# Kernel optimization log

Measured on AMD Instinct MI355X. Metric: run time of the kernel, lower is better.

The kernel has to match this reference:

```python
import jax, jax.numpy as jnp
import numpy as np

B, T, C = 2, 2048, 1024
H, HS = 16, 64
THETA = 10000.0


def _rope_tables(seq_len, dim, dtype):
    inv_freq = 1.0 / (THETA ** (jnp.arange(0, dim, 2, dtype=jnp.float32) / dim))
    t = jnp.arange(seq_len, dtype=jnp.float32)
    freqs = t[:, None] * inv_freq[None, :]          # [T, dim/2]
    emb = jnp.concatenate([freqs, freqs], axis=-1)  # [T, dim]
    return jnp.cos(emb).astype(dtype), jnp.sin(emb).astype(dtype)


def _rotate_half(x):
    x1, x2 = jnp.split(x, 2, axis=-1)
    return jnp.concatenate([-x2, x1], axis=-1)


def setup_inputs() -> dict:
    key = jax.random.key(0)
    ks = jax.random.split(key, 9)
    s = 0.02
    return {
        "q_x": jax.random.normal(ks[0], (B, T, C), dtype=jnp.float32),
        "wq": jax.random.normal(ks[1], (C, H * HS), dtype=jnp.float32) * s,
        "bq": jnp.zeros((H * HS,), dtype=jnp.float32),
        "wk": jax.random.normal(ks[2], (C, H * HS), dtype=jnp.float32) * s,
        "bk": jnp.zeros((H * HS,), dtype=jnp.float32),
        "wv": jax.random.normal(ks[3], (C, H * HS), dtype=jnp.float32) * s,
        "bv": jnp.zeros((H * HS,), dtype=jnp.float32),
        "wc": jax.random.normal(ks[4], (H * HS, C), dtype=jnp.float32) * s,
        "bc": jnp.zeros((C,), dtype=jnp.float32),
    }


def reference(q_x, wq, bq, wk, bk, wv, bv, wc, bc):
    b, t, _ = q_x.shape
    # Q/K/V projections -> [B, H, T, HS]
    q = (q_x @ wq + bq).reshape(b, t, H, HS).transpose(0, 2, 1, 3)
    k = (q_x @ wk + bk).reshape(b, t, H, HS).transpose(0, 2, 1, 3)
    v = (q_x @ wv + bv).reshape(b, t, H, HS).transpose(0, 2, 1, 3)
    # RoPE (concat-half rotation)
    cos, sin = _rope_tables(t, HS, q.dtype)  # [T, HS]
    q = q * cos + _rotate_half(q) * sin
    k = k * cos + _rotate_half(k) * sin
    # Naive causal attention
    scale = 1.0 / np.sqrt(HS)
    att = jnp.einsum("bhqd,bhkd->bhqk", q, k) * scale
    mask = jnp.tril(jnp.ones((t, t), dtype=bool))
    att = jnp.where(mask, att, -jnp.inf)
    att = jax.nn.softmax(att, axis=-1)
    y = jnp.einsum("bhqk,bhkd->bhqd", att, v)
    y = y.transpose(0, 2, 1, 3).reshape(b, t, H * HS)
    return y @ wc + bc
```

## Files before the change

### kernel.cpp

```cpp
#include <hip/hip_runtime.h>

#define B_  2
#define T_  2048
#define C_  1024
#define H_  16
#define HS_ 64
#define M_  4096
#define N_  1024
#define K_  1024

typedef float floatx4 __attribute__((ext_vector_type(4)));
typedef short bf16x8  __attribute__((ext_vector_type(8)));

__device__ __forceinline__ float bf2f(unsigned short u) {
    return __uint_as_float(((unsigned int)u) << 16);
}
__device__ __forceinline__ unsigned short f2bf(float f) {
    unsigned int u = __float_as_uint(f);
    return (unsigned short)((u + 0x7fffu + ((u >> 16) & 1u)) >> 16);
}
__device__ __forceinline__ unsigned int pack2(float a, float b) {
    return (unsigned int)f2bf(a) | ((unsigned int)f2bf(b) << 16);
}
__device__ __forceinline__ void async16(const unsigned short* g, unsigned short* l) {
    __builtin_amdgcn_global_load_lds(
        (const __attribute__((address_space(1))) unsigned int*)g,
        (__attribute__((address_space(3))) unsigned int*)l, 16, 0, 0);
}

__global__ __launch_bounds__(256) void convert_x(const float* __restrict__ x,
                                                 unsigned short* __restrict__ xb)
{
    const size_t i = ((size_t)blockIdx.x * 256 + threadIdx.x) * 4;
    const float4 v = *(const float4*)(x + i);
    ushort4 st;
    st.x = f2bf(v.x); st.y = f2bf(v.y); st.z = f2bf(v.z); st.w = f2bf(v.w);
    *(ushort4*)(xb + i) = st;
}

__global__ __launch_bounds__(256) void transpose_w(
    const float* __restrict__ w0, const float* __restrict__ w1,
    const float* __restrict__ w2, const float* __restrict__ w3,
    unsigned short* __restrict__ wTall)
{
    __shared__ float tile[64][65];
    const int z = blockIdx.z;
    const float* w = (z == 0) ? w0 : (z == 1) ? w1 : (z == 2) ? w2 : w3;
    unsigned short* wT = wTall + ((size_t)z << 20);

    const int n0 = blockIdx.x * 64, k0 = blockIdx.y * 64;
    const int t = threadIdx.x;
    const int r = t >> 2, cq = (t & 3) * 16;

    const float4* src = (const float4*)(w + (size_t)(k0 + r) * N_ + n0 + cq);
    const float4 v0 = src[0], v1 = src[1], v2 = src[2], v3 = src[3];
    tile[r][cq+0]=v0.x; tile[r][cq+1]=v0.y; tile[r][cq+2]=v0.z; tile[r][cq+3]=v0.w;
    tile[r][cq+4]=v1.x; tile[r][cq+5]=v1.y; tile[r][cq+6]=v1.z; tile[r][cq+7]=v1.w;
    tile[r][cq+8]=v2.x; tile[r][cq+9]=v2.y; tile[r][cq+10]=v2.z; tile[r][cq+11]=v2.w;
    tile[r][cq+12]=v3.x; tile[r][cq+13]=v3.y; tile[r][cq+14]=v3.z; tile[r][cq+15]=v3.w;
    __syncthreads();

    const int rn = t >> 2, ck = (t & 3) * 16;
    unsigned int o[8];
#pragma unroll
    for (int ii = 0; ii < 8; ii++)
        o[ii] = pack2(tile[ck + 2*ii][rn], tile[ck + 2*ii + 1][rn]);
    unsigned short* dst = wT + (size_t)(n0 + rn) * K_ + k0 + ck;
    *(uint4*)dst       = make_uint4(o[0], o[1], o[2], o[3]);
    *(uint4*)(dst + 8) = make_uint4(o[4], o[5], o[6], o[7]);
}

__global__ __launch_bounds__(256) void qkv_gemm(
    const unsigned short* __restrict__ xb, const unsigned short* __restrict__ wT,
    const float* __restrict__ bq, const float* __restrict__ bk,
    const float* __restrict__ bv,
    unsigned short* __restrict__ qb, unsigned short* __restrict__ kb,
    unsigned short* __restrict__ vb)
{
    __shared__ unsigned short As[128 * 32];
    __shared__ unsigned short Bs[128 * 32];

    const int tid  = threadIdx.x;
    const int lane = tid & 63;
    const int wave = tid >> 6;
    const int p  = blockIdx.x >> 3;
    const int n0 = (blockIdx.x & 7) * 128;
    const int m0 = blockIdx.y * 128;
    const float* bias = (p == 0) ? bq : (p == 1) ? bk : bv;

    const int lrow = lane >> 2, lch = (lane & 3) * 8;
    const unsigned short* ag0 = xb + (size_t)(m0 + wave * 32 + lrow) * K_ + lch;
    const unsigned short* ag1 = ag0 + (size_t)16 * K_;
    const unsigned short* wb  = wT + ((size_t)p << 20);
    const unsigned short* bg0 = wb + (size_t)(n0 + wave * 32 + lrow) * K_ + lch;
    const unsigned short* bg1 = bg0 + (size_t)16 * K_;
    unsigned short* lA0 = &As[(wave * 32) * 32];
    unsigned short* lA1 = &As[(wave * 32 + 16) * 32];
    unsigned short* lB0 = &Bs[(wave * 32) * 32];
    unsigned short* lB1 = &Bs[(wave * 32 + 16) * 32];

    const int fr = lane & 15;
    const int fk = (lane >> 4) * 8;
    const int wr = wave >> 1, wc = wave & 1;

    floatx4 acc[4][4];
#pragma unroll
    for (int i = 0; i < 4; i++)
#pragma unroll
        for (int j = 0; j < 4; j++) acc[i][j] = (floatx4){0.f, 0.f, 0.f, 0.f};

    for (int k0 = 0; k0 < K_; k0 += 32) {
        __syncthreads();
        async16(ag0 + k0, lA0);
        async16(ag1 + k0, lA1);
        async16(bg0 + k0, lB0);
        async16(bg1 + k0, lB1);
        __syncthreads();

        bf16x8 af[4], bfr[4];
#pragma unroll
        for (int i = 0; i < 4; i++)
            af[i] = *(const bf16x8*)&As[(wr * 64 + i * 16 + fr) * 32 + fk];
#pragma unroll
        for (int j = 0; j < 4; j++)
            bfr[j] = *(const bf16x8*)&Bs[(wc * 64 + j * 16 + fr) * 32 + fk];
#pragma unroll
        for (int i = 0; i < 4; i++)
#pragma unroll
            for (int j = 0; j < 4; j++)
                acc[i][j] = __builtin_amdgcn_mfma_f32_16x16x32_bf16(
                    af[i], bfr[j], acc[i][j], 0, 0, 0);
    }

    const int rbase = (lane >> 4) * 4;
    if (p == 2) {
#pragma unroll
        for (int j = 0; j < 4; j++) {
            const int col = n0 + wc * 64 + j * 16 + fr;
            const float bz = bias[col];
            const int h = col >> 6, d = col & 63;
#pragma unroll
            for (int i = 0; i < 4; i++) {
                const int row0 = m0 + wr * 64 + i * 16 + rbase;
                const int bb = row0 >> 11, tt = row0 & 2047;
                ushort4 st;
                st.x = f2bf(acc[i][j][0] + bz);
                st.y = f2bf(acc[i][j][1] + bz);
                st.z = f2bf(acc[i][j][2] + bz);
                st.w = f2bf(acc[i][j][3] + bz);
                *(ushort4*)&vb[((size_t)(bb * H_ + h) * HS_ + d) * T_ + tt] = st;
            }
        }
    } else {
        unsigned short* out = (p == 0) ? qb : kb;
#pragma unroll
        for (int j = 0; j < 4; j++) {
            const int col = n0 + wc * 64 + j * 16 + fr;
            const float bz = bias[col];
            const int h = col >> 6, d = col & 63;
#pragma unroll
            for (int i = 0; i < 4; i++) {
#pragma unroll
                for (int pr = 0; pr < 4; pr++) {
                    const int row = m0 + wr * 64 + i * 16 + rbase + pr;
                    const int bb = row >> 11, tt = row & 2047;
                    out[((size_t)(bb * H_ + h) * T_ + tt) * HS_ + d] =
                        f2bf(acc[i][j][pr] + bz);
                }
            }
        }
    }
}

__global__ __launch_bounds__(256) void rope_kernel(unsigned short* __restrict__ qb,
                                                   unsigned short* __restrict__ kb)
{
    const int idx = blockIdx.x * 256 + threadIdx.x;
    const int d  = idx & 31;
    const int t  = (idx >> 5) & (T_ - 1);
    const int bh = idx >> 16;
    const size_t base = ((size_t)bh * T_ + t) * HS_;

    const float inv_freq = powf(10000.0f, -(float)d * (1.0f / 32.0f));
    float s, c;
    sincosf((float)t * inv_freq, &s, &c);

    {
        float x1 = bf2f(qb[base + d]), x2 = bf2f(qb[base + d + 32]);
        qb[base + d]      = f2bf((x1 * c - x2 * s) * 0.125f);
        qb[base + d + 32] = f2bf((x2 * c + x1 * s) * 0.125f);
    }
    {
        float x1 = bf2f(kb[base + d]), x2 = bf2f(kb[base + d + 32]);
        kb[base + d]      = f2bf(x1 * c - x2 * s);
        kb[base + d + 32] = f2bf(x2 * c + x1 * s);
    }
}

__global__ __launch_bounds__(256) void attn_kernel(
    const unsigned short* __restrict__ qb, const unsigned short* __restrict__ kb,
    const unsigned short* __restrict__ vt, unsigned short* __restrict__ yb)
{
    __shared__ unsigned short Ks[64 * 64];
    __shared__ unsigned short Vs[64 * 64];
    __shared__ unsigned short Ps[4][16 * 64];

    const int bh = blockIdx.x;
    const int b = bh >> 4, h = bh & 15;
    const int qt = blockIdx.y;
    const int r0 = qt * 64;
    const int tid  = threadIdx.x;
    const int lane = tid & 63;
    const int wave = tid >> 6;
    const int l4   = lane & 15;
    const int quad = lane >> 4;

    const int qrow_g = r0 + wave * 16 + l4;

    bf16x8 qf[2];
    {
        const unsigned short* qp = qb + ((size_t)bh * T_ + qrow_g) * HS_ + quad * 8;
        qf[0] = *(const bf16x8*)(qp);
        qf[1] = *(const bf16x8*)(qp + 32);
    }

    floatx4 o[4];
#pragma unroll
    for (int g = 0; g < 4; g++) o[g] = (floatx4){0.f, 0.f, 0.f, 0.f};
    float m = -1e30f, l = 0.f;

    const int srow = tid >> 2;
    const int sc16 = (tid & 3) * 16;
    const int ssw  = (srow & 7) * 8;
    const int psw  = (l4 & 7) * 8;

    for (int kt = 0; kt <= qt; kt++) {
        const unsigned short* kp = kb + ((size_t)bh * T_ + kt * 64 + srow) * HS_ + sc16;
        const uint4 k0 = *(const uint4*)kp;
        const uint4 k1 = *(const uint4*)(kp + 8);
        const unsigned short* vp = vt + ((size_t)(bh * 64 + srow)) * T_ + kt * 64 + sc16;
        const uint4 v0 = *(const uint4*)vp;
        const uint4 v1 = *(const uint4*)(vp + 8);

        __syncthreads();
        *(uint4*)&Ks[srow * 64 + ( sc16      ^ ssw)] = k0;
        *(uint4*)&Ks[srow * 64 + ((sc16 + 8) ^ ssw)] = k1;
        *(uint4*)&Vs[srow * 64 + ( sc16      ^ ssw)] = v0;
        *(uint4*)&Vs[srow * 64 + ((sc16 + 8) ^ ssw)] = v1;
        __syncthreads();

        floatx4 sf[4];
#pragma unroll
        for (int mg = 0; mg < 4; mg++) {
            const int key = mg * 16 + l4;
            const int ksw = (key & 7) * 8;
            const bf16x8 a0 = *(const bf16x8*)&Ks[key * 64 + ( (quad * 8)       ^ ksw)];
            const bf16x8 a1 = *(const bf16x8*)&Ks[key * 64 + (((quad * 8) + 32) ^ ksw)];
            floatx4 z = (floatx4){0.f, 0.f, 0.f, 0.f};
            z = __builtin_amdgcn_mfma_f32_16x16x32_bf16(a0, qf[0], z, 0, 0, 0);
            z = __builtin_amdgcn_mfma_f32_16x16x32_bf16(a1, qf[1], z, 0, 0, 0);
            sf[mg] = z;
        }

        if (kt == qt) {
#pragma unroll
            for (int mg = 0; mg < 4; mg++)
#pragma unroll
                for (int r = 0; r < 4; r++)
                    if (kt * 64 + 16 * mg + quad * 4 + r > qrow_g)
                        sf[mg][r] = -1e30f;
        }

        float tm = sf[0][0];
#pragma unroll
        for (int mg = 0; mg < 4; mg++)
#pragma unroll
            for (int r = 0; r < 4; r++) tm = fmaxf(tm, sf[mg][r]);
        tm = fmaxf(tm, __shfl_xor(tm, 16));
        tm = fmaxf(tm, __shfl_xor(tm, 32));
        const float mnew  = fmaxf(m, tm);
        const float alpha = __expf(m - mnew);

        float p[4][4];
        float ps = 0.f;
#pragma unroll
        for (int mg = 0; mg < 4; mg++)
#pragma unroll
            for (int r = 0; r < 4; r++) {
                p[mg][r] = __expf(sf[mg][r] - mnew);
                ps += p[mg][r];
            }
        ps += __shfl_xor(ps, 16);
        ps += __shfl_xor(ps, 32);
        l = l * alpha + ps;
        m = mnew;
#pragma unroll
        for (int g = 0; g < 4; g++) {
            o[g][0] *= alpha; o[g][1] *= alpha;
            o[g][2] *= alpha; o[g][3] *= alpha;
        }

#pragma unroll
        for (int mg = 0; mg < 4; mg++) {
            const int kb4 = 16 * mg + quad * 4;
            const int off = ((kb4 & ~7) ^ psw) | (kb4 & 7);
            uint2 w;
            w.x = pack2(p[mg][0], p[mg][1]);
            w.y = pack2(p[mg][2], p[mg][3]);
            *(uint2*)&Ps[wave][l4 * 64 + off] = w;
        }

        const bf16x8 pf0 = *(const bf16x8*)&Ps[wave][l4 * 64 + ( (quad * 8)       ^ psw)];
        const bf16x8 pf1 = *(const bf16x8*)&Ps[wave][l4 * 64 + (((quad * 8) + 32) ^ psw)];
#pragma unroll
        for (int g = 0; g < 4; g++) {
            const int vd  = g * 16 + l4;
            const int vsw = (vd & 7) * 8;
            const bf16x8 va0 = *(const bf16x8*)&Vs[vd * 64 + ( (quad * 8)       ^ vsw)];
            const bf16x8 va1 = *(const bf16x8*)&Vs[vd * 64 + (((quad * 8) + 32) ^ vsw)];
            o[g] = __builtin_amdgcn_mfma_f32_16x16x32_bf16(va0, pf0, o[g], 0, 0, 0);
            o[g] = __builtin_amdgcn_mfma_f32_16x16x32_bf16(va1, pf1, o[g], 0, 0, 0);
        }
    }

    const float invl = 1.f / l;
    unsigned short* yrow = yb + ((size_t)(b * T_ + qrow_g) * H_ + h) * HS_;
#pragma unroll
    for (int g = 0; g < 4; g++) {
        ushort4 st;
        st.x = f2bf(o[g][0] * invl);
        st.y = f2bf(o[g][1] * invl);
        st.z = f2bf(o[g][2] * invl);
        st.w = f2bf(o[g][3] * invl);
        *(ushort4*)&yrow[16 * g + quad * 4] = st;
    }
}

__global__ __launch_bounds__(256) void out_gemm(
    const unsigned short* __restrict__ A, const unsigned short* __restrict__ wcT,
    const float* __restrict__ bias, float* __restrict__ out)
{
    __shared__ unsigned short As[128 * 32];
    __shared__ unsigned short Bs[128 * 32];

    const int tid  = threadIdx.x;
    const int lane = tid & 63;
    const int wave = tid >> 6;
    const int n0 = blockIdx.x * 128;
    const int m0 = blockIdx.y * 128;

    const int lrow = lane >> 2, lch = (lane & 3) * 8;
    const unsigned short* ag0 = A + (size_t)(m0 + wave * 32 + lrow) * K_ + lch;
    const unsigned short* ag1 = ag0 + (size_t)16 * K_;
    const unsigned short* bg0 = wcT + (size_t)(n0 + wave * 32 + lrow) * K_ + lch;
    const unsigned short* bg1 = bg0 + (size_t)16 * K_;
    unsigned short* lA0 = &As[(wave * 32) * 32];
    unsigned short* lA1 = &As[(wave * 32 + 16) * 32];
    unsigned short* lB0 = &Bs[(wave * 32) * 32];
    unsigned short* lB1 = &Bs[(wave * 32 + 16) * 32];

    const int fr = lane & 15;
    const int fk = (lane >> 4) * 8;
    const int wr = wave >> 1, wc = wave & 1;

    floatx4 acc[4][4];
#pragma unroll
    for (int i = 0; i < 4; i++)
#pragma unroll
        for (int j = 0; j < 4; j++) acc[i][j] = (floatx4){0.f, 0.f, 0.f, 0.f};

    for (int k0 = 0; k0 < K_; k0 += 32) {
        __syncthreads();
        async16(ag0 + k0, lA0);
        async16(ag1 + k0, lA1);
        async16(bg0 + k0, lB0);
        async16(bg1 + k0, lB1);
        __syncthreads();

        bf16x8 af[4], bfr[4];
#pragma unroll
        for (int i = 0; i < 4; i++)
            af[i] = *(const bf16x8*)&As[(wr * 64 + i * 16 + fr) * 32 + fk];
#pragma unroll
        for (int j = 0; j < 4; j++)
            bfr[j] = *(const bf16x8*)&Bs[(wc * 64 + j * 16 + fr) * 32 + fk];
#pragma unroll
        for (int i = 0; i < 4; i++)
#pragma unroll
            for (int j = 0; j < 4; j++)
                acc[i][j] = __builtin_amdgcn_mfma_f32_16x16x32_bf16(
                    af[i], bfr[j], acc[i][j], 0, 0, 0);
    }

    const int rbase = (lane >> 4) * 4;
#pragma unroll
    for (int j = 0; j < 4; j++) {
        const int col = n0 + wc * 64 + j * 16 + fr;
        const float bz = bias[col];
#pragma unroll
        for (int i = 0; i < 4; i++) {
#pragma unroll
            for (int pr = 0; pr < 4; pr++) {
                const int row = m0 + wr * 64 + i * 16 + rbase + pr;
                out[(size_t)row * N_ + col] = acc[i][j][pr] + bz;
            }
        }
    }
}

extern "C" void kernel_launch(void* const* d_in, const int* in_sizes, int n_in,
                              void* d_out, int out_size, void* d_ws, size_t ws_size,
                              hipStream_t stream) {
    const float* x  = (const float*)d_in[0];
    const float* wq = (const float*)d_in[1];
    const float* bq = (const float*)d_in[2];
    const float* wk = (const float*)d_in[3];
    const float* bk = (const float*)d_in[4];
    const float* wv = (const float*)d_in[5];
    const float* bv = (const float*)d_in[6];
    const float* wc = (const float*)d_in[7];
    const float* bc = (const float*)d_in[8];
    float* out = (float*)d_out;

    unsigned short* ws  = (unsigned short*)d_ws;
    unsigned short* qb  = ws;
    unsigned short* kb  = ws + (size_t)4194304;
    unsigned short* vb  = ws + (size_t)8388608;
    unsigned short* yb  = ws + (size_t)12582912;
    unsigned short* xb  = ws + (size_t)16777216;
    unsigned short* wT  = ws + (size_t)20971520;
    unsigned short* wcT = wT + ((size_t)3 << 20);

    convert_x<<<4096, 256, 0, stream>>>(x, xb);
    transpose_w<<<dim3(16, 16, 4), 256, 0, stream>>>(wq, wk, wv, wc, wT);
    qkv_gemm<<<dim3(24, 32), 256, 0, stream>>>(xb, wT, bq, bk, bv, qb, kb, vb);
    rope_kernel<<<(B_ * H_ * T_ * 32) / 256, 256, 0, stream>>>(qb, kb);
    attn_kernel<<<dim3(32, 32), 256, 0, stream>>>(qb, kb, vb, yb);
    out_gemm<<<dim3(8, 32), 256, 0, stream>>>(yb, wcT, bc, out);
}
```

Baseline: 231.3 us.

## Fuse RoPE into QKV epilogue, double-buffer attention K/V, reverse tile order

```diff
diff --git a/kernel.cpp b/kernel.cpp
--- a/kernel.cpp
+++ b/kernel.cpp
@@ -133,12 +133,13 @@
     }
 
     const int rbase = (lane >> 4) * 4;
+    const int h = (n0 + wc * 64) >> 6;
     if (p == 2) {
 #pragma unroll
         for (int j = 0; j < 4; j++) {
             const int col = n0 + wc * 64 + j * 16 + fr;
             const float bz = bias[col];
-            const int h = col >> 6, d = col & 63;
+            const int d = col & 63;
 #pragma unroll
             for (int i = 0; i < 4; i++) {
                 const int row0 = m0 + wr * 64 + i * 16 + rbase;
@@ -153,47 +154,34 @@
         }
     } else {
         unsigned short* out = (p == 0) ? qb : kb;
-#pragma unroll
-        for (int j = 0; j < 4; j++) {
-            const int col = n0 + wc * 64 + j * 16 + fr;
-            const float bz = bias[col];
-            const int h = col >> 6, d = col & 63;
-#pragma unroll
-            for (int i = 0; i < 4; i++) {
-#pragma unroll
-                for (int pr = 0; pr < 4; pr++) {
-                    const int row = m0 + wr * 64 + i * 16 + rbase + pr;
-                    const int bb = row >> 11, tt = row & 2047;
-                    out[((size_t)(bb * H_ + h) * T_ + tt) * HS_ + d] =
-                        f2bf(acc[i][j][pr] + bz);
-                }
+        const float qsc = (p == 0) ? 0.18033688011111772f : 1.0f;
+        const float bz0 = bias[n0 + wc * 64 + fr];
+        const float bz1 = bias[n0 + wc * 64 + 16 + fr];
+        const float bz2 = bias[n0 + wc * 64 + 32 + fr];
+        const float bz3 = bias[n0 + wc * 64 + 48 + fr];
+        const float nl = -0.41524101186279297f;
+        const float if0 = exp2f((float)fr * nl);
+        const float if1 = exp2f((float)(fr + 16) * nl);
+#pragma unroll
+        for (int i = 0; i < 4; i++) {
+#pragma unroll
+            for (int pr = 0; pr < 4; pr++) {
+                const int row = m0 + wr * 64 + i * 16 + rbase + pr;
+                const int bb = row >> 11, tt = row & 2047;
+                float s0, c0, s1, c1;
+                __sincosf((float)tt * if0, &s0, &c0);
+                __sincosf((float)tt * if1, &s1, &c1);
+                const float v0 = acc[i][0][pr] + bz0;
+                const float v1 = acc[i][1][pr] + bz1;
+                const float v2 = acc[i][2][pr] + bz2;
+                const float v3 = acc[i][3][pr] + bz3;
+                unsigned short* ob = out + ((size_t)(bb * H_ + h) * T_ + tt) * HS_ + fr;
+                ob[0]  = f2bf((v0 * c0 - v2 * s0) * qsc);
+                ob[16] = f2bf((v1 * c1 - v3 * s1) * qsc);
+                ob[32] = f2bf((v2 * c0 + v0 * s0) * qsc);
+                ob[48] = f2bf((v3 * c1 + v1 * s1) * qsc);
             }
         }
-    }
-}
-
-__global__ __launch_bounds__(256) void rope_kernel(unsigned short* __restrict__ qb,
-                                                   unsigned short* __restrict__ kb)
-{
-    const int idx = blockIdx.x * 256 + threadIdx.x;
-    const int d  = idx & 31;
-    const int t  = (idx >> 5) & (T_ - 1);
-    const int bh = idx >> 16;
-    const size_t base = ((size_t)bh * T_ + t) * HS_;
-
-    const float inv_freq = powf(10000.0f, -(float)d * (1.0f / 32.0f));
-    float s, c;
-    sincosf((float)t * inv_freq, &s, &c);
-
-    {
-        float x1 = bf2f(qb[base + d]), x2 = bf2f(qb[base + d + 32]);
-        qb[base + d]      = f2bf((x1 * c - x2 * s) * 0.125f);
-        qb[base + d + 32] = f2bf((x2 * c + x1 * s) * 0.125f);
-    }
-    {
-        float x1 = bf2f(kb[base + d]), x2 = bf2f(kb[base + d + 32]);
-        kb[base + d]      = f2bf(x1 * c - x2 * s);
-        kb[base + d + 32] = f2bf(x2 * c + x1 * s);
     }
 }
 
@@ -201,13 +189,13 @@
     const unsigned short* __restrict__ qb, const unsigned short* __restrict__ kb,
     const unsigned short* __restrict__ vt, unsigned short* __restrict__ yb)
 {
-    __shared__ unsigned short Ks[64 * 64];
-    __shared__ unsigned short Vs[64 * 64];
+    __shared__ unsigned short Ks[2][64 * 64];
+    __shared__ unsigned short Vs[2][64 * 64];
     __shared__ unsigned short Ps[4][16 * 64];
 
     const int bh = blockIdx.x;
     const int b = bh >> 4, h = bh & 15;
-    const int qt = blockIdx.y;
+    const int qt = (int)gridDim.y - 1 - blockIdx.y;
     const int r0 = qt * 64;
     const int tid  = threadIdx.x;
     const int lane = tid & 63;
@@ -234,19 +222,28 @@
     const int ssw  = (srow & 7) * 8;
     const int psw  = (l4 & 7) * 8;
 
+    const unsigned short* kp = kb + ((size_t)bh * T_ + srow) * HS_ + sc16;
+    const unsigned short* vp = vt + ((size_t)(bh * 64 + srow)) * T_ + sc16;
+
+    uint4 rk0 = *(const uint4*)kp;
+    uint4 rk1 = *(const uint4*)(kp + 8);
+    uint4 rv0 = *(const uint4*)vp;
+    uint4 rv1 = *(const uint4*)(vp + 8);
+    *(uint4*)&Ks[0][srow * 64 + ( sc16      ^ ssw)] = rk0;
+    *(uint4*)&Ks[0][srow * 64 + ((sc16 + 8) ^ ssw)] = rk1;
+    *(uint4*)&Vs[0][srow * 64 + ( sc16      ^ ssw)] = rv0;
+    *(uint4*)&Vs[0][srow * 64 + ((sc16 + 8) ^ ssw)] = rv1;
+
     for (int kt = 0; kt <= qt; kt++) {
-        const unsigned short* kp = kb + ((size_t)bh * T_ + kt * 64 + srow) * HS_ + sc16;
-        const uint4 k0 = *(const uint4*)kp;
-        const uint4 k1 = *(const uint4*)(kp + 8);
-        const unsigned short* vp = vt + ((size_t)(bh * 64 + srow)) * T_ + kt * 64 + sc16;
-        const uint4 v0 = *(const uint4*)vp;
-        const uint4 v1 = *(const uint4*)(vp + 8);
-
-        __syncthreads();
-        *(uint4*)&Ks[srow * 64 + ( sc16      ^ ssw)] = k0;
-        *(uint4*)&Ks[srow * 64 + ((sc16 + 8) ^ ssw)] = k1;
-        *(uint4*)&Vs[srow * 64 + ( sc16      ^ ssw)] = v0;
-        *(uint4*)&Vs[srow * 64 + ((sc16 + 8) ^ ssw)] = v1;
+        const int cur = kt & 1;
+        if (kt < qt) {
+            const unsigned short* kpn = kp + (size_t)(kt + 1) * (64 * HS_);
+            const unsigned short* vpn = vp + (kt + 1) * 64;
+            rk0 = *(const uint4*)kpn;
+            rk1 = *(const uint4*)(kpn + 8);
+            rv0 = *(const uint4*)vpn;
+            rv1 = *(const uint4*)(vpn + 8);
+        }
         __syncthreads();
 
         floatx4 sf[4];
@@ -254,8 +251,8 @@
         for (int mg = 0; mg < 4; mg++) {
             const int key = mg * 16 + l4;
             const int ksw = (key & 7) * 8;
-            const bf16x8 a0 = *(const bf16x8*)&Ks[key * 64 + ( (quad * 8)       ^ ksw)];
-            const bf16x8 a1 = *(const bf16x8*)&Ks[key * 64 + (((quad * 8) + 32) ^ ksw)];
+            const bf16x8 a0 = *(const bf16x8*)&Ks[cur][key * 64 + ( (quad * 8)       ^ ksw)];
+            const bf16x8 a1 = *(const bf16x8*)&Ks[cur][key * 64 + (((quad * 8) + 32) ^ ksw)];
             floatx4 z = (floatx4){0.f, 0.f, 0.f, 0.f};
             z = __builtin_amdgcn_mfma_f32_16x16x32_bf16(a0, qf[0], z, 0, 0, 0);
             z = __builtin_amdgcn_mfma_f32_16x16x32_bf16(a1, qf[1], z, 0, 0, 0);
@@ -279,7 +276,7 @@
         tm = fmaxf(tm, __shfl_xor(tm, 16));
         tm = fmaxf(tm, __shfl_xor(tm, 32));
         const float mnew  = fmaxf(m, tm);
-        const float alpha = __expf(m - mnew);
+        const float alpha = exp2f(m - mnew);
 
         float p[4][4];
         float ps = 0.f;
@@ -287,7 +284,7 @@
         for (int mg = 0; mg < 4; mg++)
 #pragma unroll
             for (int r = 0; r < 4; r++) {
-                p[mg][r] = __expf(sf[mg][r] - mnew);
+                p[mg][r] = exp2f(sf[mg][r] - mnew);
                 ps += p[mg][r];
             }
         ps += __shfl_xor(ps, 16);
@@ -316,10 +313,18 @@
         for (int g = 0; g < 4; g++) {
             const int vd  = g * 16 + l4;
             const int vsw = (vd & 7) * 8;
-            const bf16x8 va0 = *(const bf16x8*)&Vs[vd * 64 + ( (quad * 8)       ^ vsw)];
-            const bf16x8 va1 = *(const bf16x8*)&Vs[vd * 64 + (((quad * 8) + 32) ^ vsw)];
+            const bf16x8 va0 = *(const bf16x8*)&Vs[cur][vd * 64 + ( (quad * 8)       ^ vsw)];
+            const bf16x8 va1 = *(const bf16x8*)&Vs[cur][vd * 64 + (((quad * 8) + 32) ^ vsw)];
             o[g] = __builtin_amdgcn_mfma_f32_16x16x32_bf16(va0, pf0, o[g], 0, 0, 0);
             o[g] = __builtin_amdgcn_mfma_f32_16x16x32_bf16(va1, pf1, o[g], 0, 0, 0);
+        }
+
+        if (kt < qt) {
+            const int nxt = cur ^ 1;
+            *(uint4*)&Ks[nxt][srow * 64 + ( sc16      ^ ssw)] = rk0;
+            *(uint4*)&Ks[nxt][srow * 64 + ((sc16 + 8) ^ ssw)] = rk1;
+            *(uint4*)&Vs[nxt][srow * 64 + ( sc16      ^ ssw)] = rv0;
+            *(uint4*)&Vs[nxt][srow * 64 + ((sc16 + 8) ^ ssw)] = rv1;
         }
     }
 
@@ -434,7 +439,6 @@
     convert_x<<<4096, 256, 0, stream>>>(x, xb);
     transpose_w<<<dim3(16, 16, 4), 256, 0, stream>>>(wq, wk, wv, wc, wT);
     qkv_gemm<<<dim3(24, 32), 256, 0, stream>>>(xb, wT, bq, bk, bv, qb, kb, vb);
-    rope_kernel<<<(B_ * H_ * T_ * 32) / 256, 256, 0, stream>>>(qb, kb);
     attn_kernel<<<dim3(32, 32), 256, 0, stream>>>(qb, kb, vb, yb);
     out_gemm<<<dim3(8, 32), 256, 0, stream>>>(yb, wcT, bc, out);
 }
```

Result: faster. 215.3 us (-6.9%).
